# Kernel tuning notes

Measured on AMD Instinct MI355X. Metric: run time of the kernel, lower is better.

The kernel has to match this reference:

```python
import jax, jax.numpy as jnp
import numpy as np

D_HEAD = 64
SCALE = D_HEAD ** 0.5


def setup_inputs() -> dict:
    key = jax.random.key(0)
    kq, kk, kv = jax.random.split(key, 3)
    shape = (32, 2048, 64)  # (N = batch*heads, HW = seq, C = d_head)
    Q = jax.random.normal(kq, shape, dtype=jnp.float32)
    K = jax.random.normal(kk, shape, dtype=jnp.float32)
    V = jax.random.normal(kv, shape, dtype=jnp.float32)
    return {"Q": Q, "K": K, "V": V}


def reference(Q, K, V):
    # logits = Q K^T / sqrt(d_head); attn = softmax(logits); out = attn V
    logits = jnp.einsum('nqc,nkc->nqk', Q, K) / SCALE  # [N, HW, HW]
    attn = jax.nn.softmax(logits, axis=-1)
    return jnp.einsum('nqk,nkc->nqc', attn, V)  # [N, HW, C]
```

## Files before the change

### kernel.cpp

```cpp
#include <hip/hip_runtime.h>
#include <cstdint>
#include <cstddef>

typedef __bf16 bf16x8 __attribute__((ext_vector_type(8)));
typedef float f32x4 __attribute__((ext_vector_type(4)));
typedef float f32x16 __attribute__((ext_vector_type(16)));
typedef short s16x8 __attribute__((ext_vector_type(8)));
typedef unsigned short u16x4 __attribute__((ext_vector_type(4)));
typedef unsigned short u16x8 __attribute__((ext_vector_type(8)));
typedef int i32x4 __attribute__((ext_vector_type(4)));

#define S_LEN 2048
#define DH    64
#define BK    64
#define NTILE (S_LEN / BK)
#define NH    32
#define QBLK  128

#if __has_builtin(__builtin_amdgcn_exp2f)
#define EXPF(x) __builtin_amdgcn_exp2f(x)
#define QSCALE 0.18033688011112043f
#else
#define EXPF(x) __expf(x)
#define QSCALE 0.125f
#endif

typedef const __attribute__((address_space(1))) void* gas_ptr;
typedef __attribute__((address_space(3))) void* las_ptr;

static __device__ __forceinline__ unsigned short f2bf(float x) {
    unsigned int u = __builtin_bit_cast(unsigned int, x);
    u += 0x7FFFu + ((u >> 16) & 1u);
    return (unsigned short)(u >> 16);
}

static __device__ __forceinline__ unsigned cvtpk(float lo, float hi) {
    unsigned r;
    asm("v_cvt_pk_bf16_f32 %0, %1, %2" : "=v"(r) : "v"(lo), "v"(hi));
    return r;
}

static __device__ __forceinline__ void swap32(int& x, int& y, int hi) {
#if __has_builtin(__builtin_amdgcn_permlane32_swap)
    (void)hi;
    auto r = __builtin_amdgcn_permlane32_swap(x, y, false, false);
    x = r[0]; y = r[1];
#else
    int px = __shfl_xor(x, 32), py = __shfl_xor(y, 32);
    int nx = hi ? py : x;
    int ny = hi ? y  : px;
    x = nx; y = ny;
#endif
}

static __device__ __forceinline__ bf16x8 mkfrag(int lo0, int lo1, int up0, int up1, int hi) {
    swap32(lo0, up0, hi);
    swap32(lo1, up1, hi);
    i32x4 f = {lo0, lo1, up0, up1};
    return __builtin_bit_cast(bf16x8, f);
}

__global__ __launch_bounds__(256) void prepass(
        const float* __restrict__ Q, const float* __restrict__ K,
        const float* __restrict__ V,
        unsigned short* __restrict__ Qf, unsigned short* __restrict__ Kf,
        unsigned short* __restrict__ Vf)
{
    __shared__ float Tl[64][68];
    const int tid = threadIdx.x;
    const int head = blockIdx.x >> 5;
    const int tile = blockIdx.x & 31;

    const size_t hoff = (size_t)head * S_LEN * DH;
    const size_t soff = hoff + (size_t)tile * 64 * DH;

    #pragma unroll
    for (int p = 0; p < 4; ++p) {
        const int idx = p * 256 + tid;
        const int row = idx >> 4, c4 = idx & 15;
        *(float4*)&Tl[row][c4 * 4] = *(const float4*)(Q + soff + (size_t)row * DH + c4 * 4);
    }
    __syncthreads();
    #pragma unroll
    for (int p = 0; p < 2; ++p) {
        const int cid = p * 256 + tid;
        const int qt_l = cid >> 8;
        const int dsub = (cid >> 6) & 3;
        const int ln   = cid & 63;
        const int row  = qt_l * 32 + (ln & 31);
        const int d0   = dsub * 16 + (ln >> 5) * 8;
        u16x8 o;
        #pragma unroll
        for (int e = 0; e < 8; ++e) o[e] = f2bf(Tl[row][d0 + e] * QSCALE);
        const size_t qtile = (size_t)tile * 2 + qt_l;
        *(u16x8*)&Qf[hoff + ((qtile * 4 + dsub) * 64 + ln) * 8] = o;
    }
    __syncthreads();

    #pragma unroll
    for (int p = 0; p < 4; ++p) {
        const int idx = p * 256 + tid;
        const int row = idx >> 4, c4 = idx & 15;
        *(float4*)&Tl[row][c4 * 4] = *(const float4*)(K + soff + (size_t)row * DH + c4 * 4);
    }
    __syncthreads();
    #pragma unroll
    for (int p = 0; p < 2; ++p) {
        const int cid = p * 256 + tid;
        const int sub = cid >> 6;
        const int ln  = cid & 63;
        const int dsub = sub >> 1, half = sub & 1;
        const int row  = half * 32 + (ln & 31);
        const int d0   = dsub * 16 + (ln >> 5) * 8;
        u16x8 o;
        #pragma unroll
        for (int e = 0; e < 8; ++e) o[e] = f2bf(Tl[row][d0 + e]);
        *(u16x8*)&Kf[hoff + (((size_t)tile * 8 + sub) * 64 + ln) * 8] = o;
    }
    __syncthreads();

    #pragma unroll
    for (int p = 0; p < 4; ++p) {
        const int idx = p * 256 + tid;
        const int row = idx >> 4, c4 = idx & 15;
        *(float4*)&Tl[row][c4 * 4] = *(const float4*)(V + soff + (size_t)row * DH + c4 * 4);
    }
    __syncthreads();
    #pragma unroll
    for (int p = 0; p < 2; ++p) {
        const int cid = p * 256 + tid;
        const int sub = cid >> 6;
        const int ln  = cid & 63;
        const int ks = sub >> 1, half = sub & 1;
        const int k0 = ks * 16 + (ln >> 5) * 8;
        const int d  = half * 32 + (ln & 31);
        u16x8 o;
        #pragma unroll
        for (int e = 0; e < 8; ++e) o[e] = f2bf(Tl[k0 + e][d]);
        *(u16x8*)&Vf[hoff + (((size_t)tile * 8 + sub) * 64 + ln) * 8] = o;
    }
}

template<int NSPLIT>
__global__ __launch_bounds__(256, 4) void sdpa32_t(
        const unsigned short* __restrict__ Qf, const unsigned short* __restrict__ Kf,
        const unsigned short* __restrict__ Vf, float* __restrict__ Out,
        float* __restrict__ lpart)
{
    __shared__ __attribute__((aligned(16))) unsigned short Kl[2][512 * 8];
    __shared__ __attribute__((aligned(16))) unsigned short Vl[2][512 * 8];

    const int tid = threadIdx.x;
    const int w   = tid >> 6;
    const int ln  = tid & 63;
    const int r31 = ln & 31;
    const int hi  = ln >> 5;

    const int nblk  = NH * 16 * NSPLIT;
    const int b2    = (blockIdx.x & 7) * (nblk / 8) + (blockIdx.x >> 3);
    const int n     = b2 / (16 * NSPLIT);
    const int rem   = b2 % (16 * NSPLIT);
    const int qt    = (NSPLIT == 2) ? (rem >> 1) : rem;
    const int half  = (NSPLIT == 2) ? (rem & 1) : 0;
    const int q0    = qt * QBLK + w * 32;

    const size_t hoff = (size_t)n * S_LEN * DH;
    const unsigned short* __restrict__ Kh = Kf + hoff;
    const unsigned short* __restrict__ Vh = Vf + hoff;

    const int qtile = qt * 4 + w;
    s16x8 qf[4];
    #pragma unroll
    for (int dsub = 0; dsub < 4; ++dsub)
        qf[dsub] = *(const s16x8*)(Qf + hoff + (((size_t)qtile * 4 + dsub) * 64 + ln) * 8);

    float l = 0.f;
    f32x16 oacc0 = {}, oacc1 = {};

    auto stage = [&](int buf, int t) {
        #pragma unroll
        for (int pass = 0; pass < 2; ++pass) {
            const int c = pass * 256 + w * 64;
            const unsigned short* gk = Kh + ((size_t)t * 512 + c + ln) * 8;
            __builtin_amdgcn_global_load_lds((gas_ptr)gk, (las_ptr)&Kl[buf][c * 8], 16, 0, 0);
            const unsigned short* gv = Vh + ((size_t)t * 512 + c + ln) * 8;
            __builtin_amdgcn_global_load_lds((gas_ptr)gv, (las_ptr)&Vl[buf][c * 8], 16, 0, 0);
        }
    };

    const int t0   = half * (NTILE / NSPLIT);
    const int tEnd = t0 + NTILE / NSPLIT;

    stage(0, t0);
    __syncthreads();

    auto body = [&](int it, int cur) {
        if (it + 1 < tEnd) stage(cur ^ 1, it + 1);

        f32x16 s0 = {}, s1 = {};
        __builtin_amdgcn_s_setprio(1);
        #pragma unroll
        for (int dsub = 0; dsub < 4; ++dsub) {
            s16x8 kf0 = *(const s16x8*)&Kl[cur][((dsub * 2 + 0) * 64 + ln) * 8];
            s16x8 kf1 = *(const s16x8*)&Kl[cur][((dsub * 2 + 1) * 64 + ln) * 8];
            s0 = __builtin_amdgcn_mfma_f32_32x32x16_bf16(
                    __builtin_bit_cast(bf16x8, kf0),
                    __builtin_bit_cast(bf16x8, qf[dsub]), s0, 0, 0, 0);
            s1 = __builtin_amdgcn_mfma_f32_32x32x16_bf16(
                    __builtin_bit_cast(bf16x8, kf1),
                    __builtin_bit_cast(bf16x8, qf[dsub]), s1, 0, 0, 0);
        }
        __builtin_amdgcn_s_setprio(0);

        #pragma unroll
        for (int i = 0; i < 16; ++i) {
            s0[i] = EXPF(s0[i]);
            s1[i] = EXPF(s1[i]);
        }
        {
            float a0 = 0.f, a1 = 0.f, a2 = 0.f, a3 = 0.f;
            #pragma unroll
            for (int i = 0; i < 16; i += 4) {
                a0 += s0[i];     a1 += s0[i + 1];
                a2 += s0[i + 2]; a3 += s0[i + 3];
            }
            #pragma unroll
            for (int i = 0; i < 16; i += 4) {
                a0 += s1[i];     a1 += s1[i + 1];
                a2 += s1[i + 2]; a3 += s1[i + 3];
            }
            l += (a0 + a1) + (a2 + a3);
        }

        unsigned wa[8], wb[8];
        #pragma unroll
        for (int i = 0; i < 8; ++i) {
            wa[i] = cvtpk(s0[2 * i], s0[2 * i + 1]);
            wb[i] = cvtpk(s1[2 * i], s1[2 * i + 1]);
        }
        bf16x8 pf[4];
        pf[0] = mkfrag(wa[0], wa[1], wa[2], wa[3], hi);
        pf[1] = mkfrag(wa[4], wa[5], wa[6], wa[7], hi);
        pf[2] = mkfrag(wb[0], wb[1], wb[2], wb[3], hi);
        pf[3] = mkfrag(wb[4], wb[5], wb[6], wb[7], hi);

        __builtin_amdgcn_s_setprio(1);
        #pragma unroll
        for (int ks = 0; ks < 4; ++ks) {
            s16x8 vf0 = *(const s16x8*)&Vl[cur][((ks * 2 + 0) * 64 + ln) * 8];
            s16x8 vf1 = *(const s16x8*)&Vl[cur][((ks * 2 + 1) * 64 + ln) * 8];
            oacc0 = __builtin_amdgcn_mfma_f32_32x32x16_bf16(
                    __builtin_bit_cast(bf16x8, vf0), pf[ks], oacc0, 0, 0, 0);
            oacc1 = __builtin_amdgcn_mfma_f32_32x32x16_bf16(
                    __builtin_bit_cast(bf16x8, vf1), pf[ks], oacc1, 0, 0, 0);
        }
        __builtin_amdgcn_s_setprio(0);

        __syncthreads();
    };

    for (int it = t0; it < tEnd; it += 2) {
        body(it, 0);
        body(it + 1, 1);
    }

    const float lt = l + __shfl_xor(l, 32);
    if (NSPLIT == 1) {
        const float inv = 1.0f / lt;
        float* Orow = Out + hoff + (size_t)(q0 + r31) * DH;
        #pragma unroll
        for (int g = 0; g < 4; ++g) {
            float4 o0 = { oacc0[4*g] * inv, oacc0[4*g+1] * inv,
                          oacc0[4*g+2] * inv, oacc0[4*g+3] * inv };
            *(float4*)&Orow[g * 8 + hi * 4] = o0;
            float4 o1 = { oacc1[4*g] * inv, oacc1[4*g+1] * inv,
                          oacc1[4*g+2] * inv, oacc1[4*g+3] * inv };
            *(float4*)&Orow[32 + g * 8 + hi * 4] = o1;
        }
    } else {
        float* Orow = Out + (((size_t)half * NH + n) * S_LEN + q0 + r31) * DH;
        #pragma unroll
        for (int g = 0; g < 4; ++g) {
            float4 o0 = { oacc0[4*g], oacc0[4*g+1], oacc0[4*g+2], oacc0[4*g+3] };
            *(float4*)&Orow[g * 8 + hi * 4] = o0;
            float4 o1 = { oacc1[4*g], oacc1[4*g+1], oacc1[4*g+2], oacc1[4*g+3] };
            *(float4*)&Orow[32 + g * 8 + hi * 4] = o1;
        }
        if (!hi) lpart[((size_t)half * NH + n) * S_LEN + q0 + r31] = lt;
    }
}

__global__ __launch_bounds__(256) void combine(
        const float* __restrict__ Opart, const float* __restrict__ lpart,
        float* __restrict__ O)
{
    const int i = blockIdx.x * 256 + threadIdx.x;
    const size_t HS4 = (size_t)NH * S_LEN * DH / 4;
    const size_t row = (size_t)i >> 4;
    const float4 a = ((const float4*)Opart)[i];
    const float4 b = ((const float4*)Opart)[i + HS4];
    const float inv = 1.0f / (lpart[row] + lpart[row + (size_t)NH * S_LEN]);
    float4 o = { (a.x + b.x) * inv, (a.y + b.y) * inv,
                 (a.z + b.z) * inv, (a.w + b.w) * inv };
    ((float4*)O)[i] = o;
}

static __device__ __forceinline__ int swz_fb(int row, int col) {
    return row * 64 + (col ^ ((row & 7) << 3));
}

__global__ __launch_bounds__(256) void sdpa_fwd_fb(
        const float* __restrict__ Q, const float* __restrict__ K,
        const float* __restrict__ V, float* __restrict__ O)
{
    __shared__ __attribute__((aligned(16))) unsigned short Klf[BK * DH];
    __shared__ __attribute__((aligned(16))) unsigned short Vtf[DH * BK];
    __shared__ __attribute__((aligned(16))) unsigned short Plf[4][16 * BK];

    const int tid = threadIdx.x;
    const int w = tid >> 6, ln = tid & 63, lg = ln >> 4, lr = ln & 15;
    const int n = blockIdx.x >> 5, qt = blockIdx.x & 31;
    const int q0 = qt * 64 + w * 16;
    const size_t hoff = (size_t)n * S_LEN * DH;
    const float *Qh = Q + hoff, *Kh = K + hoff, *Vh = V + hoff;
    float* Oh = O + hoff;

    s16x8 qf[2];
    #pragma unroll
    for (int t = 0; t < 2; ++t) {
        const float* src = Qh + (size_t)(q0 + lr) * DH + t * 32 + lg * 8;
        float4 a = *(const float4*)(src);
        float4 b = *(const float4*)(src + 4);
        s16x8 v;
        v[0] = (short)f2bf(a.x * 0.125f); v[1] = (short)f2bf(a.y * 0.125f);
        v[2] = (short)f2bf(a.z * 0.125f); v[3] = (short)f2bf(a.w * 0.125f);
        v[4] = (short)f2bf(b.x * 0.125f); v[5] = (short)f2bf(b.y * 0.125f);
        v[6] = (short)f2bf(b.z * 0.125f); v[7] = (short)f2bf(b.w * 0.125f);
        qf[t] = v;
    }
    float mrow[4] = {-INFINITY, -INFINITY, -INFINITY, -INFINITY};
    float lrow[4] = {0.f, 0.f, 0.f, 0.f};
    f32x4 oacc[4];
    #pragma unroll
    for (int nn = 0; nn < 4; ++nn) oacc[nn] = (f32x4){0.f, 0.f, 0.f, 0.f};

    for (int it = 0; it < NTILE; ++it) {
        const int k0 = it * BK;
        __syncthreads();
        #pragma unroll
        for (int r4 = 0; r4 < 4; ++r4) {
            const int lin = tid + 256 * r4;
            const int row = lin >> 4, c4 = lin & 15;
            float4 kv = *(const float4*)(Kh + (size_t)(k0 + row) * DH + c4 * 4);
            u16x4 kb;
            kb[0] = f2bf(kv.x); kb[1] = f2bf(kv.y); kb[2] = f2bf(kv.z); kb[3] = f2bf(kv.w);
            *(u16x4*)&Klf[swz_fb(row, c4 * 4)] = kb;
            float4 vv = *(const float4*)(Vh + (size_t)(k0 + row) * DH + c4 * 4);
            const float vals[4] = {vv.x, vv.y, vv.z, vv.w};
            #pragma unroll
            for (int ii = 0; ii < 4; ++ii) Vtf[swz_fb(c4 * 4 + ii, row)] = f2bf(vals[ii]);
        }
        __syncthreads();
        f32x4 sacc[4];
        #pragma unroll
        for (int kt = 0; kt < 4; ++kt) {
            f32x4 acc = (f32x4){0.f, 0.f, 0.f, 0.f};
            #pragma unroll
            for (int t = 0; t < 2; ++t) {
                s16x8 kf = *(const s16x8*)&Klf[swz_fb(kt * 16 + lr, t * 32 + lg * 8)];
                acc = __builtin_amdgcn_mfma_f32_16x16x32_bf16(
                        __builtin_bit_cast(bf16x8, qf[t]),
                        __builtin_bit_cast(bf16x8, kf), acc, 0, 0, 0);
            }
            sacc[kt] = acc;
        }
        float alpha[4];
        #pragma unroll
        for (int j = 0; j < 4; ++j) {
            float v = fmaxf(fmaxf(sacc[0][j], sacc[1][j]), fmaxf(sacc[2][j], sacc[3][j]));
            #pragma unroll
            for (int off = 1; off < 16; off <<= 1) v = fmaxf(v, __shfl_xor(v, off));
            const float mn = fmaxf(mrow[j], v);
            alpha[j] = __expf(mrow[j] - mn);
            mrow[j] = mn;
        }
        float psum[4] = {0.f, 0.f, 0.f, 0.f};
        #pragma unroll
        for (int kt = 0; kt < 4; ++kt) {
            #pragma unroll
            for (int j = 0; j < 4; ++j) {
                const float p = __expf(sacc[kt][j] - mrow[j]);
                const unsigned short pb = f2bf(p);
                unsigned int pu = ((unsigned int)pb) << 16;
                psum[j] += __builtin_bit_cast(float, pu);
                Plf[w][swz_fb(lg * 4 + j, kt * 16 + lr)] = pb;
            }
        }
        #pragma unroll
        for (int j = 0; j < 4; ++j) {
            float s = psum[j];
            #pragma unroll
            for (int off = 1; off < 16; off <<= 1) s += __shfl_xor(s, off);
            lrow[j] = lrow[j] * alpha[j] + s;
        }
        #pragma unroll
        for (int nn = 0; nn < 4; ++nn) {
            #pragma unroll
            for (int j = 0; j < 4; ++j) oacc[nn][j] *= alpha[j];
        }
        #pragma unroll
        for (int t = 0; t < 2; ++t) {
            s16x8 pf = *(const s16x8*)&Plf[w][swz_fb(lr, t * 32 + lg * 8)];
            #pragma unroll
            for (int nn = 0; nn < 4; ++nn) {
                s16x8 vf = *(const s16x8*)&Vtf[swz_fb(nn * 16 + lr, t * 32 + lg * 8)];
                oacc[nn] = __builtin_amdgcn_mfma_f32_16x16x32_bf16(
                        __builtin_bit_cast(bf16x8, pf),
                        __builtin_bit_cast(bf16x8, vf), oacc[nn], 0, 0, 0);
            }
        }
    }
    #pragma unroll
    for (int j = 0; j < 4; ++j) {
        const float inv = 1.0f / lrow[j];
        #pragma unroll
        for (int nn = 0; nn < 4; ++nn)
            Oh[(size_t)(q0 + lg * 4 + j) * DH + nn * 16 + lr] = oacc[nn][j] * inv;
    }
}

extern "C" void kernel_launch(void* const* d_in, const int* in_sizes, int n_in,
                              void* d_out, int out_size, void* d_ws, size_t ws_size,
                              hipStream_t stream) {
    const float* Q = (const float*)d_in[0];
    const float* K = (const float*)d_in[1];
    const float* V = (const float*)d_in[2];
    float* O = (float*)d_out;

    const size_t elems    = (size_t)NH * S_LEN * DH;
    const size_t bf_bytes = elems * 2;
    const size_t opart_b  = 2 * elems * sizeof(float);
    const size_t lpart_b  = 2 * (size_t)NH * S_LEN * sizeof(float);
    const size_t need_split = 3 * bf_bytes + opart_b + lpart_b;

    unsigned short* Qf = (unsigned short*)d_ws;
    unsigned short* Kf = Qf + elems;
    unsigned short* Vf = Kf + elems;

    if (ws_size >= need_split) {
        float* Opart = (float*)((char*)d_ws + 3 * bf_bytes);
        float* lpart = (float*)((char*)d_ws + 3 * bf_bytes + opart_b);
        prepass<<<NH * 32, 256, 0, stream>>>(Q, K, V, Qf, Kf, Vf);
        sdpa32_t<2><<<NH * 16 * 2, 256, 0, stream>>>(Qf, Kf, Vf, Opart, lpart);
        combine<<<(int)(elems / 4 / 256), 256, 0, stream>>>(Opart, lpart, O);
    } else if (ws_size >= 3 * bf_bytes) {
        prepass<<<NH * 32, 256, 0, stream>>>(Q, K, V, Qf, Kf, Vf);
        sdpa32_t<1><<<NH * 16, 256, 0, stream>>>(Qf, Kf, Vf, O, nullptr);
    } else {
        sdpa_fwd_fb<<<NH * (S_LEN / 64), 256, 0, stream>>>(Q, K, V, O);
    }
}
```

Before: 68.46 us.

## Process two query tiles per wave and convert Q inside attention kernel

```diff
diff --git a/kernel.cpp b/kernel.cpp
--- a/kernel.cpp
+++ b/kernel.cpp
@@ -15,7 +15,6 @@
 #define BK    64
 #define NTILE (S_LEN / BK)
 #define NH    32
-#define QBLK  128
 
 #if __has_builtin(__builtin_amdgcn_exp2f)
 #define EXPF(x) __builtin_amdgcn_exp2f(x)
@@ -60,11 +59,9 @@
     return __builtin_bit_cast(bf16x8, f);
 }
 
-__global__ __launch_bounds__(256) void prepass(
-        const float* __restrict__ Q, const float* __restrict__ K,
-        const float* __restrict__ V,
-        unsigned short* __restrict__ Qf, unsigned short* __restrict__ Kf,
-        unsigned short* __restrict__ Vf)
+__global__ __launch_bounds__(256) void prepass_kv(
+        const float* __restrict__ K, const float* __restrict__ V,
+        unsigned short* __restrict__ Kf, unsigned short* __restrict__ Vf)
 {
     __shared__ float Tl[64][68];
     const int tid = threadIdx.x;
@@ -73,29 +70,6 @@
 
     const size_t hoff = (size_t)head * S_LEN * DH;
     const size_t soff = hoff + (size_t)tile * 64 * DH;
-
-    #pragma unroll
-    for (int p = 0; p < 4; ++p) {
-        const int idx = p * 256 + tid;
-        const int row = idx >> 4, c4 = idx & 15;
-        *(float4*)&Tl[row][c4 * 4] = *(const float4*)(Q + soff + (size_t)row * DH + c4 * 4);
-    }
-    __syncthreads();
-    #pragma unroll
-    for (int p = 0; p < 2; ++p) {
-        const int cid = p * 256 + tid;
-        const int qt_l = cid >> 8;
-        const int dsub = (cid >> 6) & 3;
-        const int ln   = cid & 63;
-        const int row  = qt_l * 32 + (ln & 31);
-        const int d0   = dsub * 16 + (ln >> 5) * 8;
-        u16x8 o;
-        #pragma unroll
-        for (int e = 0; e < 8; ++e) o[e] = f2bf(Tl[row][d0 + e] * QSCALE);
-        const size_t qtile = (size_t)tile * 2 + qt_l;
-        *(u16x8*)&Qf[hoff + ((qtile * 4 + dsub) * 64 + ln) * 8] = o;
-    }
-    __syncthreads();
 
     #pragma unroll
     for (int p = 0; p < 4; ++p) {
@@ -142,8 +116,8 @@
 }
 
 template<int NSPLIT>
-__global__ __launch_bounds__(256, 4) void sdpa32_t(
-        const unsigned short* __restrict__ Qf, const unsigned short* __restrict__ Kf,
+__global__ __launch_bounds__(256, 2) void sdpa64_t(
+        const float* __restrict__ Qg, const unsigned short* __restrict__ Kf,
         const unsigned short* __restrict__ Vf, float* __restrict__ Out,
         float* __restrict__ lpart)
 {
@@ -156,26 +130,45 @@
     const int r31 = ln & 31;
     const int hi  = ln >> 5;
 
-    const int nblk  = NH * 16 * NSPLIT;
-    const int b2    = (blockIdx.x & 7) * (nblk / 8) + (blockIdx.x >> 3);
-    const int n     = b2 / (16 * NSPLIT);
-    const int rem   = b2 % (16 * NSPLIT);
-    const int qt    = (NSPLIT == 2) ? (rem >> 1) : rem;
-    const int half  = (NSPLIT == 2) ? (rem & 1) : 0;
-    const int q0    = qt * QBLK + w * 32;
+    const int nblk = NH * 8 * NSPLIT;
+    const int b2   = (blockIdx.x & 7) * (nblk / 8) + (blockIdx.x >> 3);
+    const int n    = b2 / (8 * NSPLIT);
+    const int rem  = b2 % (8 * NSPLIT);
+    const int qt   = (NSPLIT == 2) ? (rem >> 1) : rem;
+    const int half = (NSPLIT == 2) ? (rem & 1) : 0;
+    const int q0A  = qt * 256 + w * 32;
+    const int q0B  = q0A + 128;
 
     const size_t hoff = (size_t)n * S_LEN * DH;
     const unsigned short* __restrict__ Kh = Kf + hoff;
     const unsigned short* __restrict__ Vh = Vf + hoff;
 
-    const int qtile = qt * 4 + w;
-    s16x8 qf[4];
-    #pragma unroll
-    for (int dsub = 0; dsub < 4; ++dsub)
-        qf[dsub] = *(const s16x8*)(Qf + hoff + (((size_t)qtile * 4 + dsub) * 64 + ln) * 8);
-
-    float l = 0.f;
-    f32x16 oacc0 = {}, oacc1 = {};
+    s16x8 qfA[4], qfB[4];
+    {
+        const float* QrA = Qg + hoff + (size_t)(q0A + r31) * DH;
+        const float* QrB = Qg + hoff + (size_t)(q0B + r31) * DH;
+        #pragma unroll
+        for (int dsub = 0; dsub < 4; ++dsub) {
+            const float* sa = QrA + dsub * 16 + hi * 8;
+            const float* sb = QrB + dsub * 16 + hi * 8;
+            float4 a0 = *(const float4*)sa, a1 = *(const float4*)(sa + 4);
+            float4 b0 = *(const float4*)sb, b1 = *(const float4*)(sb + 4);
+            s16x8 va, vb;
+            va[0] = (short)f2bf(a0.x * QSCALE); va[1] = (short)f2bf(a0.y * QSCALE);
+            va[2] = (short)f2bf(a0.z * QSCALE); va[3] = (short)f2bf(a0.w * QSCALE);
+            va[4] = (short)f2bf(a1.x * QSCALE); va[5] = (short)f2bf(a1.y * QSCALE);
+            va[6] = (short)f2bf(a1.z * QSCALE); va[7] = (short)f2bf(a1.w * QSCALE);
+            vb[0] = (short)f2bf(b0.x * QSCALE); vb[1] = (short)f2bf(b0.y * QSCALE);
+            vb[2] = (short)f2bf(b0.z * QSCALE); vb[3] = (short)f2bf(b0.w * QSCALE);
+            vb[4] = (short)f2bf(b1.x * QSCALE); vb[5] = (short)f2bf(b1.y * QSCALE);
+            vb[6] = (short)f2bf(b1.z * QSCALE); vb[7] = (short)f2bf(b1.w * QSCALE);
+            qfA[dsub] = va;
+            qfB[dsub] = vb;
+        }
+    }
+
+    float lA = 0.f, lB = 0.f;
+    f32x16 oA0 = {}, oA1 = {}, oB0 = {}, oB1 = {};
 
     auto stage = [&](int buf, int t) {
         #pragma unroll
@@ -197,62 +190,100 @@
     auto body = [&](int it, int cur) {
         if (it + 1 < tEnd) stage(cur ^ 1, it + 1);
 
-        f32x16 s0 = {}, s1 = {};
+        f32x16 sA0 = {}, sA1 = {}, sB0 = {}, sB1 = {};
         __builtin_amdgcn_s_setprio(1);
         #pragma unroll
         for (int dsub = 0; dsub < 4; ++dsub) {
             s16x8 kf0 = *(const s16x8*)&Kl[cur][((dsub * 2 + 0) * 64 + ln) * 8];
             s16x8 kf1 = *(const s16x8*)&Kl[cur][((dsub * 2 + 1) * 64 + ln) * 8];
-            s0 = __builtin_amdgcn_mfma_f32_32x32x16_bf16(
+            sA0 = __builtin_amdgcn_mfma_f32_32x32x16_bf16(
                     __builtin_bit_cast(bf16x8, kf0),
-                    __builtin_bit_cast(bf16x8, qf[dsub]), s0, 0, 0, 0);
-            s1 = __builtin_amdgcn_mfma_f32_32x32x16_bf16(
+                    __builtin_bit_cast(bf16x8, qfA[dsub]), sA0, 0, 0, 0);
+            sA1 = __builtin_amdgcn_mfma_f32_32x32x16_bf16(
                     __builtin_bit_cast(bf16x8, kf1),
-                    __builtin_bit_cast(bf16x8, qf[dsub]), s1, 0, 0, 0);
+                    __builtin_bit_cast(bf16x8, qfA[dsub]), sA1, 0, 0, 0);
+            sB0 = __builtin_amdgcn_mfma_f32_32x32x16_bf16(
+                    __builtin_bit_cast(bf16x8, kf0),
+                    __builtin_bit_cast(bf16x8, qfB[dsub]), sB0, 0, 0, 0);
+            sB1 = __builtin_amdgcn_mfma_f32_32x32x16_bf16(
+                    __builtin_bit_cast(bf16x8, kf1),
+                    __builtin_bit_cast(bf16x8, qfB[dsub]), sB1, 0, 0, 0);
         }
         __builtin_amdgcn_s_setprio(0);
 
         #pragma unroll
         for (int i = 0; i < 16; ++i) {
-            s0[i] = EXPF(s0[i]);
-            s1[i] = EXPF(s1[i]);
+            sA0[i] = EXPF(sA0[i]);
+            sA1[i] = EXPF(sA1[i]);
         }
         {
             float a0 = 0.f, a1 = 0.f, a2 = 0.f, a3 = 0.f;
             #pragma unroll
             for (int i = 0; i < 16; i += 4) {
-                a0 += s0[i];     a1 += s0[i + 1];
-                a2 += s0[i + 2]; a3 += s0[i + 3];
-            }
+                a0 += sA0[i];     a1 += sA0[i + 1];
+                a2 += sA0[i + 2]; a3 += sA0[i + 3];
+                a0 += sA1[i];     a1 += sA1[i + 1];
+                a2 += sA1[i + 2]; a3 += sA1[i + 3];
+            }
+            lA += (a0 + a1) + (a2 + a3);
+        }
+        bf16x8 pfA[4];
+        {
+            unsigned wa[8], wb[8];
+            #pragma unroll
+            for (int i = 0; i < 8; ++i) {
+                wa[i] = cvtpk(sA0[2 * i], sA0[2 * i + 1]);
+                wb[i] = cvtpk(sA1[2 * i], sA1[2 * i + 1]);
+            }
+            pfA[0] = mkfrag(wa[0], wa[1], wa[2], wa[3], hi);
+            pfA[1] = mkfrag(wa[4], wa[5], wa[6], wa[7], hi);
+            pfA[2] = mkfrag(wb[0], wb[1], wb[2], wb[3], hi);
+            pfA[3] = mkfrag(wb[4], wb[5], wb[6], wb[7], hi);
+        }
+
+        #pragma unroll
+        for (int i = 0; i < 16; ++i) {
+            sB0[i] = EXPF(sB0[i]);
+            sB1[i] = EXPF(sB1[i]);
+        }
+        {
+            float a0 = 0.f, a1 = 0.f, a2 = 0.f, a3 = 0.f;
             #pragma unroll
             for (int i = 0; i < 16; i += 4) {
-                a0 += s1[i];     a1 += s1[i + 1];
-                a2 += s1[i + 2]; a3 += s1[i + 3];
-            }
-            l += (a0 + a1) + (a2 + a3);
-        }
-
-        unsigned wa[8], wb[8];
-        #pragma unroll
-        for (int i = 0; i < 8; ++i) {
-            wa[i] = cvtpk(s0[2 * i], s0[2 * i + 1]);
-            wb[i] = cvtpk(s1[2 * i], s1[2 * i + 1]);
-        }
-        bf16x8 pf[4];
-        pf[0] = mkfrag(wa[0], wa[1], wa[2], wa[3], hi);
-        pf[1] = mkfrag(wa[4], wa[5], wa[6], wa[7], hi);
-        pf[2] = mkfrag(wb[0], wb[1], wb[2], wb[3], hi);
-        pf[3] = mkfrag(wb[4], wb[5], wb[6], wb[7], hi);
+                a0 += sB0[i];     a1 += sB0[i + 1];
+                a2 += sB0[i + 2]; a3 += sB0[i + 3];
+                a0 += sB1[i];     a1 += sB1[i + 1];
+                a2 += sB1[i + 2]; a3 += sB1[i + 3];
+            }
+            lB += (a0 + a1) + (a2 + a3);
+        }
+        bf16x8 pfB[4];
+        {
+            unsigned wa[8], wb[8];
+            #pragma unroll
+            for (int i = 0; i < 8; ++i) {
+                wa[i] = cvtpk(sB0[2 * i], sB0[2 * i + 1]);
+                wb[i] = cvtpk(sB1[2 * i], sB1[2 * i + 1]);
+            }
+            pfB[0] = mkfrag(wa[0], wa[1], wa[2], wa[3], hi);
+            pfB[1] = mkfrag(wa[4], wa[5], wa[6], wa[7], hi);
+            pfB[2] = mkfrag(wb[0], wb[1], wb[2], wb[3], hi);
+            pfB[3] = mkfrag(wb[4], wb[5], wb[6], wb[7], hi);
+        }
 
         __builtin_amdgcn_s_setprio(1);
         #pragma unroll
         for (int ks = 0; ks < 4; ++ks) {
             s16x8 vf0 = *(const s16x8*)&Vl[cur][((ks * 2 + 0) * 64 + ln) * 8];
             s16x8 vf1 = *(const s16x8*)&Vl[cur][((ks * 2 + 1) * 64 + ln) * 8];
-            oacc0 = __builtin_amdgcn_mfma_f32_32x32x16_bf16(
-                    __builtin_bit_cast(bf16x8, vf0), pf[ks], oacc0, 0, 0, 0);
-            oacc1 = __builtin_amdgcn_mfma_f32_32x32x16_bf16(
-                    __builtin_bit_cast(bf16x8, vf1), pf[ks], oacc1, 0, 0, 0);
+            oA0 = __builtin_amdgcn_mfma_f32_32x32x16_bf16(
+                    __builtin_bit_cast(bf16x8, vf0), pfA[ks], oA0, 0, 0, 0);
+            oA1 = __builtin_amdgcn_mfma_f32_32x32x16_bf16(
+                    __builtin_bit_cast(bf16x8, vf1), pfA[ks], oA1, 0, 0, 0);
+            oB0 = __builtin_amdgcn_mfma_f32_32x32x16_bf16(
+                    __builtin_bit_cast(bf16x8, vf0), pfB[ks], oB0, 0, 0, 0);
+            oB1 = __builtin_amdgcn_mfma_f32_32x32x16_bf16(
+                    __builtin_bit_cast(bf16x8, vf1), pfB[ks], oB1, 0, 0, 0);
         }
         __builtin_amdgcn_s_setprio(0);
 
@@ -264,29 +295,42 @@
         body(it + 1, 1);
     }
 
-    const float lt = l + __shfl_xor(l, 32);
+    const float ltA = lA + __shfl_xor(lA, 32);
+    const float ltB = lB + __shfl_xor(lB, 32);
     if (NSPLIT == 1) {
-        const float inv = 1.0f / lt;
-        float* Orow = Out + hoff + (size_t)(q0 + r31) * DH;
+        const float invA = 1.0f / ltA, invB = 1.0f / ltB;
+        float* OrA = Out + hoff + (size_t)(q0A + r31) * DH;
+        float* OrB = Out + hoff + (size_t)(q0B + r31) * DH;
         #pragma unroll
         for (int g = 0; g < 4; ++g) {
-            float4 o0 = { oacc0[4*g] * inv, oacc0[4*g+1] * inv,
-                          oacc0[4*g+2] * inv, oacc0[4*g+3] * inv };
-            *(float4*)&Orow[g * 8 + hi * 4] = o0;
-            float4 o1 = { oacc1[4*g] * inv, oacc1[4*g+1] * inv,
-                          oacc1[4*g+2] * inv, oacc1[4*g+3] * inv };
-            *(float4*)&Orow[32 + g * 8 + hi * 4] = o1;
+            float4 a0 = { oA0[4*g] * invA, oA0[4*g+1] * invA, oA0[4*g+2] * invA, oA0[4*g+3] * invA };
+            *(float4*)&OrA[g * 8 + hi * 4] = a0;
+            float4 a1 = { oA1[4*g] * invA, oA1[4*g+1] * invA, oA1[4*g+2] * invA, oA1[4*g+3] * invA };
+            *(float4*)&OrA[32 + g * 8 + hi * 4] = a1;
+            float4 b0 = { oB0[4*g] * invB, oB0[4*g+1] * invB, oB0[4*g+2] * invB, oB0[4*g+3] * invB };
+            *(float4*)&OrB[g * 8 + hi * 4] = b0;
+            float4 b1 = { oB1[4*g] * invB, oB1[4*g+1] * invB, oB1[4*g+2] * invB, oB1[4*g+3] * invB };
+            *(float4*)&OrB[32 + g * 8 + hi * 4] = b1;
         }
     } else {
-        float* Orow = Out + (((size_t)half * NH + n) * S_LEN + q0 + r31) * DH;
+        const size_t pbase = ((size_t)half * NH + n) * S_LEN;
+        float* OrA = Out + (pbase + q0A + r31) * DH;
+        float* OrB = Out + (pbase + q0B + r31) * DH;
         #pragma unroll
         for (int g = 0; g < 4; ++g) {
-            float4 o0 = { oacc0[4*g], oacc0[4*g+1], oacc0[4*g+2], oacc0[4*g+3] };
-            *(float4*)&Orow[g * 8 + hi * 4] = o0;
-            float4 o1 = { oacc1[4*g], oacc1[4*g+1], oacc1[4*g+2], oacc1[4*g+3] };
-            *(float4*)&Orow[32 + g * 8 + hi * 4] = o1;
-        }
-        if (!hi) lpart[((size_t)half * NH + n) * S_LEN + q0 + r31] = lt;
+            float4 a0 = { oA0[4*g], oA0[4*g+1], oA0[4*g+2], oA0[4*g+3] };
+            *(float4*)&OrA[g * 8 + hi * 4] = a0;
+            float4 a1 = { oA1[4*g], oA1[4*g+1], oA1[4*g+2], oA1[4*g+3] };
+            *(float4*)&OrA[32 + g * 8 + hi * 4] = a1;
+            float4 b0 = { oB0[4*g], oB0[4*g+1], oB0[4*g+2], oB0[4*g+3] };
+            *(float4*)&OrB[g * 8 + hi * 4] = b0;
+            float4 b1 = { oB1[4*g], oB1[4*g+1], oB1[4*g+2], oB1[4*g+3] };
+            *(float4*)&OrB[32 + g * 8 + hi * 4] = b1;
+        }
+        if (!hi) {
+            lpart[pbase + q0A + r31] = ltA;
+            lpart[pbase + q0B + r31] = ltB;
+        }
     }
 }
 
@@ -441,21 +485,20 @@
     const size_t bf_bytes = elems * 2;
     const size_t opart_b  = 2 * elems * sizeof(float);
     const size_t lpart_b  = 2 * (size_t)NH * S_LEN * sizeof(float);
-    const size_t need_split = 3 * bf_bytes + opart_b + lpart_b;
-
-    unsigned short* Qf = (unsigned short*)d_ws;
-    unsigned short* Kf = Qf + elems;
+    const size_t need_split = 2 * bf_bytes + opart_b + lpart_b;
+
+    unsigned short* Kf = (unsigned short*)d_ws;
     unsigned short* Vf = Kf + elems;
 
     if (ws_size >= need_split) {
-        float* Opart = (float*)((char*)d_ws + 3 * bf_bytes);
-        float* lpart = (float*)((char*)d_ws + 3 * bf_bytes + opart_b);
-        prepass<<<NH * 32, 256, 0, stream>>>(Q, K, V, Qf, Kf, Vf);
-        sdpa32_t<2><<<NH * 16 * 2, 256, 0, stream>>>(Qf, Kf, Vf, Opart, lpart);
+        float* Opart = (float*)((char*)d_ws + 2 * bf_bytes);
+        float* lpart = (float*)((char*)d_ws + 2 * bf_bytes + opart_b);
+        prepass_kv<<<NH * 32, 256, 0, stream>>>(K, V, Kf, Vf);
+        sdpa64_t<2><<<NH * 8 * 2, 256, 0, stream>>>(Q, Kf, Vf, Opart, lpart);
         combine<<<(int)(elems / 4 / 256), 256, 0, stream>>>(Opart, lpart, O);
-    } else if (ws_size >= 3 * bf_bytes) {
-        prepass<<<NH * 32, 256, 0, stream>>>(Q, K, V, Qf, Kf, Vf);
-        sdpa32_t<1><<<NH * 16, 256, 0, stream>>>(Qf, Kf, Vf, O, nullptr);
+    } else if (ws_size >= 2 * bf_bytes) {
+        prepass_kv<<<NH * 32, 256, 0, stream>>>(K, V, Kf, Vf);
+        sdpa64_t<1><<<NH * 8, 256, 0, stream>>>(Q, Kf, Vf, O, nullptr);
     } else {
         sdpa_fwd_fb<<<NH * (S_LEN / 64), 256, 0, stream>>>(Q, K, V, O);
     }
```

Result: faster. 64.04 us (-6.5%).

## Fuse KV-split combine into attention kernel and convert Q in-kernel

Applied to the files above, without the earlier changes.

```diff
diff --git a/kernel.cpp b/kernel.cpp
--- a/kernel.cpp
+++ b/kernel.cpp
@@ -15,7 +15,6 @@
 #define BK    64
 #define NTILE (S_LEN / BK)
 #define NH    32
-#define QBLK  128
 
 #if __has_builtin(__builtin_amdgcn_exp2f)
 #define EXPF(x) __builtin_amdgcn_exp2f(x)
@@ -60,11 +59,9 @@
     return __builtin_bit_cast(bf16x8, f);
 }
 
-__global__ __launch_bounds__(256) void prepass(
-        const float* __restrict__ Q, const float* __restrict__ K,
-        const float* __restrict__ V,
-        unsigned short* __restrict__ Qf, unsigned short* __restrict__ Kf,
-        unsigned short* __restrict__ Vf)
+__global__ __launch_bounds__(256) void prepass_kv(
+        const float* __restrict__ K, const float* __restrict__ V,
+        unsigned short* __restrict__ Kf, unsigned short* __restrict__ Vf)
 {
     __shared__ float Tl[64][68];
     const int tid = threadIdx.x;
@@ -73,29 +70,6 @@
 
     const size_t hoff = (size_t)head * S_LEN * DH;
     const size_t soff = hoff + (size_t)tile * 64 * DH;
-
-    #pragma unroll
-    for (int p = 0; p < 4; ++p) {
-        const int idx = p * 256 + tid;
-        const int row = idx >> 4, c4 = idx & 15;
-        *(float4*)&Tl[row][c4 * 4] = *(const float4*)(Q + soff + (size_t)row * DH + c4 * 4);
-    }
-    __syncthreads();
-    #pragma unroll
-    for (int p = 0; p < 2; ++p) {
-        const int cid = p * 256 + tid;
-        const int qt_l = cid >> 8;
-        const int dsub = (cid >> 6) & 3;
-        const int ln   = cid & 63;
-        const int row  = qt_l * 32 + (ln & 31);
-        const int d0   = dsub * 16 + (ln >> 5) * 8;
-        u16x8 o;
-        #pragma unroll
-        for (int e = 0; e < 8; ++e) o[e] = f2bf(Tl[row][d0 + e] * QSCALE);
-        const size_t qtile = (size_t)tile * 2 + qt_l;
-        *(u16x8*)&Qf[hoff + ((qtile * 4 + dsub) * 64 + ln) * 8] = o;
-    }
-    __syncthreads();
 
     #pragma unroll
     for (int p = 0; p < 4; ++p) {
@@ -141,38 +115,47 @@
     }
 }
 
-template<int NSPLIT>
-__global__ __launch_bounds__(256, 4) void sdpa32_t(
-        const unsigned short* __restrict__ Qf, const unsigned short* __restrict__ Kf,
-        const unsigned short* __restrict__ Vf, float* __restrict__ Out,
-        float* __restrict__ lpart)
+__global__ __launch_bounds__(512, 4) void sdpa_fused(
+        const float* __restrict__ Qg, const unsigned short* __restrict__ Kf,
+        const unsigned short* __restrict__ Vf, float* __restrict__ O)
 {
-    __shared__ __attribute__((aligned(16))) unsigned short Kl[2][512 * 8];
-    __shared__ __attribute__((aligned(16))) unsigned short Vl[2][512 * 8];
+    __shared__ __attribute__((aligned(16))) unsigned short SH[32768];
 
     const int tid = threadIdx.x;
-    const int w   = tid >> 6;
+    const int w8  = tid >> 6;
+    const int grp = w8 >> 2;
+    const int w   = w8 & 3;
     const int ln  = tid & 63;
     const int r31 = ln & 31;
     const int hi  = ln >> 5;
 
-    const int nblk  = NH * 16 * NSPLIT;
-    const int b2    = (blockIdx.x & 7) * (nblk / 8) + (blockIdx.x >> 3);
-    const int n     = b2 / (16 * NSPLIT);
-    const int rem   = b2 % (16 * NSPLIT);
-    const int qt    = (NSPLIT == 2) ? (rem >> 1) : rem;
-    const int half  = (NSPLIT == 2) ? (rem & 1) : 0;
-    const int q0    = qt * QBLK + w * 32;
+    const int b2 = (blockIdx.x & 7) * 64 + (blockIdx.x >> 3);
+    const int n  = b2 >> 4;
+    const int qt = b2 & 15;
+    const int q0 = qt * 128 + w * 32;
 
     const size_t hoff = (size_t)n * S_LEN * DH;
     const unsigned short* __restrict__ Kh = Kf + hoff;
     const unsigned short* __restrict__ Vh = Vf + hoff;
 
-    const int qtile = qt * 4 + w;
+    const int kbase = grp * 8192;
+    const int vbase = 16384 + grp * 8192;
+
     s16x8 qf[4];
-    #pragma unroll
-    for (int dsub = 0; dsub < 4; ++dsub)
-        qf[dsub] = *(const s16x8*)(Qf + hoff + (((size_t)qtile * 4 + dsub) * 64 + ln) * 8);
+    {
+        const float* Qr = Qg + hoff + (size_t)(q0 + r31) * DH;
+        #pragma unroll
+        for (int dsub = 0; dsub < 4; ++dsub) {
+            const float* s = Qr + dsub * 16 + hi * 8;
+            float4 a0 = *(const float4*)s, a1 = *(const float4*)(s + 4);
+            s16x8 v;
+            v[0] = (short)f2bf(a0.x * QSCALE); v[1] = (short)f2bf(a0.y * QSCALE);
+            v[2] = (short)f2bf(a0.z * QSCALE); v[3] = (short)f2bf(a0.w * QSCALE);
+            v[4] = (short)f2bf(a1.x * QSCALE); v[5] = (short)f2bf(a1.y * QSCALE);
+            v[6] = (short)f2bf(a1.z * QSCALE); v[7] = (short)f2bf(a1.w * QSCALE);
+            qf[dsub] = v;
+        }
+    }
 
     float l = 0.f;
     f32x16 oacc0 = {}, oacc1 = {};
@@ -182,27 +165,28 @@
         for (int pass = 0; pass < 2; ++pass) {
             const int c = pass * 256 + w * 64;
             const unsigned short* gk = Kh + ((size_t)t * 512 + c + ln) * 8;
-            __builtin_amdgcn_global_load_lds((gas_ptr)gk, (las_ptr)&Kl[buf][c * 8], 16, 0, 0);
+            __builtin_amdgcn_global_load_lds((gas_ptr)gk,
+                    (las_ptr)&SH[kbase + buf * 4096 + c * 8], 16, 0, 0);
             const unsigned short* gv = Vh + ((size_t)t * 512 + c + ln) * 8;
-            __builtin_amdgcn_global_load_lds((gas_ptr)gv, (las_ptr)&Vl[buf][c * 8], 16, 0, 0);
+            __builtin_amdgcn_global_load_lds((gas_ptr)gv,
+                    (las_ptr)&SH[vbase + buf * 4096 + c * 8], 16, 0, 0);
         }
     };
 
-    const int t0   = half * (NTILE / NSPLIT);
-    const int tEnd = t0 + NTILE / NSPLIT;
+    const int t0 = grp * (NTILE / 2);
 
     stage(0, t0);
     __syncthreads();
 
     auto body = [&](int it, int cur) {
-        if (it + 1 < tEnd) stage(cur ^ 1, it + 1);
+        if (it + 1 < NTILE / 2) stage(cur ^ 1, t0 + it + 1);
 
         f32x16 s0 = {}, s1 = {};
         __builtin_amdgcn_s_setprio(1);
         #pragma unroll
         for (int dsub = 0; dsub < 4; ++dsub) {
-            s16x8 kf0 = *(const s16x8*)&Kl[cur][((dsub * 2 + 0) * 64 + ln) * 8];
-            s16x8 kf1 = *(const s16x8*)&Kl[cur][((dsub * 2 + 1) * 64 + ln) * 8];
+            s16x8 kf0 = *(const s16x8*)&SH[kbase + cur * 4096 + ((dsub * 2 + 0) * 64 + ln) * 8];
+            s16x8 kf1 = *(const s16x8*)&SH[kbase + cur * 4096 + ((dsub * 2 + 1) * 64 + ln) * 8];
             s0 = __builtin_amdgcn_mfma_f32_32x32x16_bf16(
                     __builtin_bit_cast(bf16x8, kf0),
                     __builtin_bit_cast(bf16x8, qf[dsub]), s0, 0, 0, 0);
@@ -223,9 +207,6 @@
             for (int i = 0; i < 16; i += 4) {
                 a0 += s0[i];     a1 += s0[i + 1];
                 a2 += s0[i + 2]; a3 += s0[i + 3];
-            }
-            #pragma unroll
-            for (int i = 0; i < 16; i += 4) {
                 a0 += s1[i];     a1 += s1[i + 1];
                 a2 += s1[i + 2]; a3 += s1[i + 3];
             }
@@ -247,8 +228,8 @@
         __builtin_amdgcn_s_setprio(1);
         #pragma unroll
         for (int ks = 0; ks < 4; ++ks) {
-            s16x8 vf0 = *(const s16x8*)&Vl[cur][((ks * 2 + 0) * 64 + ln) * 8];
-            s16x8 vf1 = *(const s16x8*)&Vl[cur][((ks * 2 + 1) * 64 + ln) * 8];
+            s16x8 vf0 = *(const s16x8*)&SH[vbase + cur * 4096 + ((ks * 2 + 0) * 64 + ln) * 8];
+            s16x8 vf1 = *(const s16x8*)&SH[vbase + cur * 4096 + ((ks * 2 + 1) * 64 + ln) * 8];
             oacc0 = __builtin_amdgcn_mfma_f32_32x32x16_bf16(
                     __builtin_bit_cast(bf16x8, vf0), pf[ks], oacc0, 0, 0, 0);
             oacc1 = __builtin_amdgcn_mfma_f32_32x32x16_bf16(
@@ -259,50 +240,42 @@
         __syncthreads();
     };
 
-    for (int it = t0; it < tEnd; it += 2) {
+    for (int it = 0; it < NTILE / 2; it += 2) {
         body(it, 0);
         body(it + 1, 1);
     }
 
     const float lt = l + __shfl_xor(l, 32);
-    if (NSPLIT == 1) {
-        const float inv = 1.0f / lt;
-        float* Orow = Out + hoff + (size_t)(q0 + r31) * DH;
+
+    float* xch = (float*)SH;
+    if (grp == 1) {
+        float* dst = xch + ((size_t)(w * 64 + ln)) * 34;
+        #pragma unroll
+        for (int i = 0; i < 16; ++i) {
+            dst[i]      = oacc0[i];
+            dst[16 + i] = oacc1[i];
+        }
+        dst[32] = lt;
+    }
+    __syncthreads();
+    if (grp == 0) {
+        const float* src = xch + ((size_t)(w * 64 + ln)) * 34;
+        const float inv = 1.0f / (lt + src[32]);
+        float* Orow = O + hoff + (size_t)(q0 + r31) * DH;
         #pragma unroll
         for (int g = 0; g < 4; ++g) {
-            float4 o0 = { oacc0[4*g] * inv, oacc0[4*g+1] * inv,
-                          oacc0[4*g+2] * inv, oacc0[4*g+3] * inv };
+            float4 o0 = { (oacc0[4*g]   + src[4*g])     * inv,
+                          (oacc0[4*g+1] + src[4*g+1])   * inv,
+                          (oacc0[4*g+2] + src[4*g+2])   * inv,
+                          (oacc0[4*g+3] + src[4*g+3])   * inv };
             *(float4*)&Orow[g * 8 + hi * 4] = o0;
-            float4 o1 = { oacc1[4*g] * inv, oacc1[4*g+1] * inv,
-                          oacc1[4*g+2] * inv, oacc1[4*g+3] * inv };
+            float4 o1 = { (oacc1[4*g]   + src[16+4*g])   * inv,
+                          (oacc1[4*g+1] + src[16+4*g+1]) * inv,
+                          (oacc1[4*g+2] + src[16+4*g+2]) * inv,
+                          (oacc1[4*g+3] + src[16+4*g+3]) * inv };
             *(float4*)&Orow[32 + g * 8 + hi * 4] = o1;
         }
-    } else {
-        float* Orow = Out + (((size_t)half * NH + n) * S_LEN + q0 + r31) * DH;
-        #pragma unroll
-        for (int g = 0; g < 4; ++g) {
-            float4 o0 = { oacc0[4*g], oacc0[4*g+1], oacc0[4*g+2], oacc0[4*g+3] };
-            *(float4*)&Orow[g * 8 + hi * 4] = o0;
-            float4 o1 = { oacc1[4*g], oacc1[4*g+1], oacc1[4*g+2], oacc1[4*g+3] };
-            *(float4*)&Orow[32 + g * 8 + hi * 4] = o1;
-        }
-        if (!hi) lpart[((size_t)half * NH + n) * S_LEN + q0 + r31] = lt;
-    }
-}
-
-__global__ __launch_bounds__(256) void combine(
-        const float* __restrict__ Opart, const float* __restrict__ lpart,
-        float* __restrict__ O)
-{
-    const int i = blockIdx.x * 256 + threadIdx.x;
-    const size_t HS4 = (size_t)NH * S_LEN * DH / 4;
-    const size_t row = (size_t)i >> 4;
-    const float4 a = ((const float4*)Opart)[i];
-    const float4 b = ((const float4*)Opart)[i + HS4];
-    const float inv = 1.0f / (lpart[row] + lpart[row + (size_t)NH * S_LEN]);
-    float4 o = { (a.x + b.x) * inv, (a.y + b.y) * inv,
-                 (a.z + b.z) * inv, (a.w + b.w) * inv };
-    ((float4*)O)[i] = o;
+    }
 }
 
 static __device__ __forceinline__ int swz_fb(int row, int col) {
@@ -439,23 +412,13 @@
 
     const size_t elems    = (size_t)NH * S_LEN * DH;
     const size_t bf_bytes = elems * 2;
-    const size_t opart_b  = 2 * elems * sizeof(float);
-    const size_t lpart_b  = 2 * (size_t)NH * S_LEN * sizeof(float);
-    const size_t need_split = 3 * bf_bytes + opart_b + lpart_b;
-
-    unsigned short* Qf = (unsigned short*)d_ws;
-    unsigned short* Kf = Qf + elems;
+
+    unsigned short* Kf = (unsigned short*)d_ws;
     unsigned short* Vf = Kf + elems;
 
-    if (ws_size >= need_split) {
-        float* Opart = (float*)((char*)d_ws + 3 * bf_bytes);
-        float* lpart = (float*)((char*)d_ws + 3 * bf_bytes + opart_b);
-        prepass<<<NH * 32, 256, 0, stream>>>(Q, K, V, Qf, Kf, Vf);
-        sdpa32_t<2><<<NH * 16 * 2, 256, 0, stream>>>(Qf, Kf, Vf, Opart, lpart);
-        combine<<<(int)(elems / 4 / 256), 256, 0, stream>>>(Opart, lpart, O);
-    } else if (ws_size >= 3 * bf_bytes) {
-        prepass<<<NH * 32, 256, 0, stream>>>(Q, K, V, Qf, Kf, Vf);
-        sdpa32_t<1><<<NH * 16, 256, 0, stream>>>(Qf, Kf, Vf, O, nullptr);
+    if (ws_size >= 2 * bf_bytes) {
+        prepass_kv<<<NH * 32, 256, 0, stream>>>(K, V, Kf, Vf);
+        sdpa_fused<<<NH * 16, 512, 0, stream>>>(Q, Kf, Vf, O);
     } else {
         sdpa_fwd_fb<<<NH * (S_LEN / 64), 256, 0, stream>>>(Q, K, V, O);
     }
```

Result: faster. 57.47 us (-16.1%).
